# Kernel tuning notes

Hardware: AMD Instinct MI355X
Metric: run time of the kernel (lower is better)

## Reference

```python
import jax, jax.numpy as jnp
import numpy as np

B, N = 1, 768
C_S, C_Z, C_H, H, P_QK, P_V = 384, 128, 16, 12, 4, 8
INF = 100000.0
EPS = 1e-8


def _points(s, w, b, rot, trans, P):
    # PointProjection: linear -> [B,N,H,3,P] -> [B,N,H,P,3] local points,
    # then global = R @ p_local + t (rigid broadcast over heads/points).
    pl = (s @ w + b).reshape(s.shape[0], s.shape[1], H, 3, P)
    pl = jnp.moveaxis(pl, -2, -1)  # [B,N,H,P,3]
    return jnp.einsum('bnij,bnhpj->bnhpi', rot, pl) + trans[:, :, None, None, :]


def setup_inputs():
    key = jax.random.key(0)
    ks = jax.random.split(key, 14)

    def lin(k, fi, fo):
        k1, k2 = jax.random.split(k)
        w = jax.random.normal(k1, (fi, fo), jnp.float32) / np.float32(np.sqrt(fi))
        b = jax.random.normal(k2, (fo,), jnp.float32) * 0.01
        return w, b

    s = jax.random.normal(ks[0], (B, N, C_S), jnp.float32)
    z = jax.random.normal(ks[1], (B, N, N, C_Z), jnp.float32)
    rot = jnp.linalg.qr(jax.random.normal(ks[2], (B, N, 3, 3), jnp.float32))[0]
    trans = jax.random.normal(ks[3], (B, N, 3), jnp.float32)
    mask = jnp.ones((B, N), jnp.float32)

    w_q, b_q = lin(ks[4], C_S, H * C_H)
    w_k, b_k = lin(ks[5], C_S, H * C_H)
    w_v, b_v = lin(ks[6], C_S, H * C_H)
    w_qp, b_qp = lin(ks[7], C_S, H * 3 * P_QK)
    w_kp, b_kp = lin(ks[8], C_S, H * 3 * P_QK)
    w_vp, b_vp = lin(ks[9], C_S, H * 3 * P_V)
    w_b, b_b = lin(ks[10], C_Z, H)
    head_weights = jax.random.normal(ks[11], (H,), jnp.float32) * 0.1
    w_o, b_o = lin(ks[12], H * (C_Z + C_H + 4 * P_V), C_S)

    return dict(s=s, z=z, rot=rot, trans=trans, mask=mask,
                w_q=w_q, b_q=b_q, w_k=w_k, b_k=b_k, w_v=w_v, b_v=b_v,
                w_qp=w_qp, b_qp=b_qp, w_kp=w_kp, b_kp=b_kp, w_vp=w_vp, b_vp=b_vp,
                w_b=w_b, b_b=b_b, head_weights=head_weights, w_o=w_o, b_o=b_o)


def reference(s, z, rot, trans, mask,
              w_q, b_q, w_k, b_k, w_v, b_v,
              w_qp, b_qp, w_kp, b_kp, w_vp, b_vp,
              w_b, b_b, head_weights, w_o, b_o):
    # per-head point weights: sqrt(2 / (9 * P_QK)) * softplus(head_weights)
    pw = np.float32(np.sqrt(2.0 / (9.0 * P_QK))) * jnp.logaddexp(head_weights, 0.0)  # [H]

    q_pts = _points(s, w_qp, b_qp, rot, trans, P_QK)  # [B,N,H,P,3]
    k_pts = _points(s, w_kp, b_kp, rot, trans, P_QK)

    # sum_p ||q_p - k_p||^2 expanded: |q|^2 + |k|^2 - 2 q.k (summed over p,xyz)
    qk_pt = jnp.einsum('bqhpc,bkhpc->bqkh', q_pts, k_pts)
    q2 = jnp.sum(q_pts * q_pts, axis=(-2, -1))  # [B,N,H]
    k2 = jnp.sum(k_pts * k_pts, axis=(-2, -1))
    pt_att = -0.5 * pw * (q2[:, :, None, :] + k2[:, None, :, :] - 2.0 * qk_pt)  # [B,Nq,Nk,H]

    q = (s @ w_q + b_q).reshape(B, N, H, C_H) * np.float32(np.sqrt(1.0 / C_H))
    k = (s @ w_k + b_k).reshape(B, N, H, C_H)
    a = pt_att + jnp.einsum('bqhc,bkhc->bqkh', q, k)
    a = a + (z @ w_b + b_b)  # pair bias [B,Nq,Nk,H]

    sq_mask = mask[:, :, None] * mask[:, None, :]
    a = a + (INF * (sq_mask - 1.0))[..., None]
    a = jax.nn.softmax(a * np.float32(np.sqrt(1.0 / 3.0)), axis=-2)  # softmax over k

    v = (s @ w_v + b_v).reshape(B, N, H, C_H)
    o = jnp.einsum('bqkh,bkhc->bqhc', a, v).reshape(B, N, H * C_H)

    v_pts = _points(s, w_vp, b_vp, rot, trans, P_V)  # [B,N,H,P,3]
    o_pt = jnp.einsum('bqkh,bkhpc->bqhpc', a, v_pts).reshape(B, N, H * P_V, 3)
    # inverse rigid: R^T @ (p - t)
    o_pt = jnp.einsum('bnji,bnpj->bnpi', rot, o_pt - trans[:, :, None, :])  # [B,N,H*P_V,3]
    o_pt_norm = jnp.sqrt(jnp.sum(o_pt * o_pt, axis=-1) + EPS)  # [B,N,H*P_V]

    o_pair = jnp.einsum('bqkh,bqkc->bqhc', a, z).reshape(B, N, H * C_Z)

    cat = jnp.concatenate(
        [o, o_pt[..., 0], o_pt[..., 1], o_pt[..., 2], o_pt_norm, o_pair], axis=-1)
    return cat @ w_o + b_o  # [B,N,C_S]
```

## Files before the change

kernel.cpp:

```cpp
#include <hip/hip_runtime.h>
#include <math.h>

#define NN 768
#define KALL 1152
#define CATD 2112
#define INF_ 100000.0f
#define PACKN (385 * KALL)

__device__ __forceinline__ float4 ld4(const float* p) { return *(const float4*)p; }

__global__ __launch_bounds__(256) void pack_kernel(
    const float* wq, const float* bq, const float* wk, const float* bk,
    const float* wv, const float* bv, const float* wqp, const float* bqp,
    const float* wkp, const float* bkp, const float* wvp, const float* bvp,
    const float* wbm, float* Wall, float* ball, float* wtr) {
  int idx = blockIdx.x * 256 + threadIdx.x;
  if (idx >= PACKN + 1536) return;
  if (idx >= PACKN) {
    int u = idx - PACKN;
    int h = u >> 7, c = u & 127;
    wtr[u] = wbm[c * 12 + h];
    return;
  }
  int kk = idx / KALL, u = idx - kk * KALL;
  const float *w, *b; int col, dim; float sc = 1.f;
  if (u < 192)      { w = wq;  b = bq;  col = u;       dim = 192; sc = 0.25f; }
  else if (u < 384) { w = wk;  b = bk;  col = u - 192; dim = 192; }
  else if (u < 576) { w = wv;  b = bv;  col = u - 384; dim = 192; }
  else if (u < 720) { w = wqp; b = bqp; col = u - 576; dim = 144; }
  else if (u < 864) { w = wkp; b = bkp; col = u - 720; dim = 144; }
  else              { w = wvp; b = bvp; col = u - 864; dim = 288; }
  if (kk < 384) Wall[kk * KALL + u] = sc * w[kk * dim + col];
  else          ball[u] = sc * b[col];
}

__global__ __launch_bounds__(256) void proj_kernel(const float* s, const float* Wall,
                                                   const float* ball, float* proj) {
  int q0 = blockIdx.x * 32, c0 = blockIdx.y * 64;
  int tid = threadIdx.x;
  int qa = q0 + (tid >> 4) * 2, qb = qa + 1;
  int c = c0 + (tid & 15) * 4;
  const float* sa = s + qa * 384;
  const float* sb = s + qb * 384;
  const float* wp = Wall + c;
  float4 acc0 = {0, 0, 0, 0}, acc1 = {0, 0, 0, 0};
#pragma unroll 4
  for (int k = 0; k < 384; k++) {
    float4 w4 = ld4(wp + k * KALL);
    float a0 = sa[k], a1 = sb[k];
    acc0.x += a0 * w4.x; acc0.y += a0 * w4.y; acc0.z += a0 * w4.z; acc0.w += a0 * w4.w;
    acc1.x += a1 * w4.x; acc1.y += a1 * w4.y; acc1.z += a1 * w4.z; acc1.w += a1 * w4.w;
  }
  float4 b4 = ld4(ball + c);
  acc0.x += b4.x; acc0.y += b4.y; acc0.z += b4.z; acc0.w += b4.w;
  acc1.x += b4.x; acc1.y += b4.y; acc1.z += b4.z; acc1.w += b4.w;
  *(float4*)(proj + (size_t)qa * KALL + c) = acc0;
  *(float4*)(proj + (size_t)qb * KALL + c) = acc1;
}

__global__ __launch_bounds__(256) void points_kernel(const float* proj, const float* rot,
                                                     const float* trans, float* qpts, float* kpts,
                                                     float* vpts, float* q2, float* k2) {
  int n = blockIdx.x, tid = threadIdx.x;
  __shared__ float sq[12], sk[12];
  if (tid < 12) { sq[tid] = 0.f; sk[tid] = 0.f; }
  __syncthreads();
  if (tid < 192) {
    const float* R = rot + n * 9;
    const float* T = trans + n * 3;
    const float* pr = proj + (size_t)n * KALL;
    int base, P; float* outp; int h; bool isq = false, isk = false;
    if (tid < 48)      { h = tid >> 2; int p = tid & 3; base = 576 + h * 12; P = 4;
                         outp = qpts + n * 144 + h * 12 + p * 3; base += p; isq = true; }
    else if (tid < 96) { int i = tid - 48; h = i >> 2; int p = i & 3; base = 720 + h * 12; P = 4;
                         outp = kpts + n * 144 + h * 12 + p * 3; base += p; isk = true; }
    else               { int i = tid - 96; h = i >> 3; int p = i & 7; base = 864 + h * 24; P = 8;
                         outp = vpts + n * 288 + h * 24 + p * 3; base += p; }
    float l0 = pr[base], l1 = pr[base + P], l2 = pr[base + 2 * P];
    float g0 = R[0] * l0 + R[1] * l1 + R[2] * l2 + T[0];
    float g1 = R[3] * l0 + R[4] * l1 + R[5] * l2 + T[1];
    float g2 = R[6] * l0 + R[7] * l1 + R[8] * l2 + T[2];
    outp[0] = g0; outp[1] = g1; outp[2] = g2;
    float ns = g0 * g0 + g1 * g1 + g2 * g2;
    if (isq) atomicAdd(&sq[h], ns);
    else if (isk) atomicAdd(&sk[h], ns);
  }
  __syncthreads();
  if (tid < 12) { q2[n * 12 + tid] = sq[tid]; k2[n * 12 + tid] = sk[tid]; }
}

__global__ __launch_bounds__(256) void bias_kernel(const float* __restrict__ z,
                                                   const float* __restrict__ wtr,
                                                   const float* __restrict__ bb,
                                                   float* __restrict__ abuf) {
  int q = blockIdx.x, k0 = blockIdx.y * 96;
  int tid = threadIdx.x;
  int lane = tid & 63;
  int wv = tid >> 6;
  int grp = lane >> 5;
  int cl = lane & 31;
  __shared__ float lsm[96 * 100];

  float4 w4[12];
#pragma unroll
  for (int h = 0; h < 12; h++) w4[h] = ld4(wtr + h * 128 + cl * 4);

  const float* zq = z + ((size_t)q * NN + k0) * 128;
  int rbase = wv * 24;
  int quad = cl >> 2, sub = cl & 3;
#pragma unroll 2
  for (int it = 0; it < 12; it++) {
    int rloc = rbase + it * 2 + grp;
    float4 z4 = ld4(zq + (size_t)rloc * 128 + cl * 4);
    float a[12];
#pragma unroll
    for (int h = 0; h < 12; h++)
      a[h] = z4.x * w4[h].x + z4.y * w4[h].y + z4.z * w4[h].z + z4.w * w4[h].w;
#pragma unroll
    for (int h = 0; h < 12; h++) {
      a[h] += __shfl_xor(a[h], 1, 64);
      a[h] += __shfl_xor(a[h], 2, 64);
    }
    bool s1 = (sub == 1), s2 = (sub == 2);
    float vx = s1 ? a[4] : (s2 ? a[8]  : a[0]);
    float vy = s1 ? a[5] : (s2 ? a[9]  : a[1]);
    float vz = s1 ? a[6] : (s2 ? a[10] : a[2]);
    float vw = s1 ? a[7] : (s2 ? a[11] : a[3]);
    if (sub < 3) {
      float* p = lsm + rloc * 100 + quad * 12 + sub * 4;
      *(float4*)p = make_float4(vx, vy, vz, vw);
    }
  }
  __syncthreads();
  for (int i = tid; i < 96 * 12; i += 256) {
    int h = i / 96, k = i - h * 96;
    const float* p = lsm + k * 100 + h;
    float ssum = bb[h];
#pragma unroll
    for (int g = 0; g < 8; g++) ssum += p[g * 12];
    abuf[((size_t)q * 12 + h) * NN + k0 + k] = ssum;
  }
}

__global__ __launch_bounds__(256) void softmax_kernel(const float* proj, const float* qpts,
                                                      const float* kpts, const float* q2,
                                                      const float* k2, const float* mask,
                                                      const float* hw, float* abuf) {
  int q0 = blockIdx.x * 8, h = blockIdx.y;
  int tid = threadIdx.x;
  __shared__ float qw[8][16], qp[8][12], q2s[8], mq[8], red[4][8], row[8], pws;
  if (tid < 128) qw[tid >> 4][tid & 15] = proj[(size_t)(q0 + (tid >> 4)) * KALL + h * 16 + (tid & 15)];
  else if (tid < 224) { int i = tid - 128; qp[i / 12][i % 12] = qpts[(q0 + i / 12) * 144 + h * 12 + i % 12]; }
  else if (tid < 232) q2s[tid - 224] = q2[(q0 + tid - 224) * 12 + h];
  else if (tid < 240) mq[tid - 232] = mask[q0 + tid - 232];
  else if (tid == 240) {
    float x = hw[h];
    pws = 0.23570226039551584f * (fmaxf(x, 0.f) + log1pf(__expf(-fabsf(x))));
  }
  __syncthreads();

  float L[3][8];
#pragma unroll
  for (int i = 0; i < 3; i++) {
    int kk = i * 256 + tid;
    float kw[16], kp[12];
    const float* kwp = proj + (size_t)kk * KALL + 192 + h * 16;
    *(float4*)(kw) = ld4(kwp); *(float4*)(kw + 4) = ld4(kwp + 4);
    *(float4*)(kw + 8) = ld4(kwp + 8); *(float4*)(kw + 12) = ld4(kwp + 12);
    const float* kpp = kpts + (size_t)kk * 144 + h * 12;
    *(float4*)(kp) = ld4(kpp); *(float4*)(kp + 4) = ld4(kpp + 4); *(float4*)(kp + 8) = ld4(kpp + 8);
    float k2v = k2[kk * 12 + h];
    float mk = mask[kk];
#pragma unroll
    for (int q = 0; q < 8; q++) {
      float4 qa = *(const float4*)&qw[q][0];
      float4 qb = *(const float4*)&qw[q][4];
      float4 qc = *(const float4*)&qw[q][8];
      float4 qd = *(const float4*)&qw[q][12];
      float4 pa = *(const float4*)&qp[q][0];
      float4 pb = *(const float4*)&qp[q][4];
      float4 pc = *(const float4*)&qp[q][8];
      float d = qa.x * kw[0] + qa.y * kw[1] + qa.z * kw[2] + qa.w * kw[3]
              + qb.x * kw[4] + qb.y * kw[5] + qb.z * kw[6] + qb.w * kw[7]
              + qc.x * kw[8] + qc.y * kw[9] + qc.z * kw[10] + qc.w * kw[11]
              + qd.x * kw[12] + qd.y * kw[13] + qd.z * kw[14] + qd.w * kw[15];
      float dp = pa.x * kp[0] + pa.y * kp[1] + pa.z * kp[2] + pa.w * kp[3]
               + pb.x * kp[4] + pb.y * kp[5] + pb.z * kp[6] + pb.w * kp[7]
               + pc.x * kp[8] + pc.y * kp[9] + pc.z * kp[10] + pc.w * kp[11];
      float bias = abuf[((size_t)(q0 + q) * 12 + h) * NN + kk];
      float val = bias + d - 0.5f * pws * (q2s[q] + k2v - 2.f * dp) + INF_ * (mq[q] * mk - 1.f);
      L[i][q] = val * 0.5773502691896258f;
    }
  }
  float m[8];
#pragma unroll
  for (int q = 0; q < 8; q++) m[q] = fmaxf(fmaxf(L[0][q], L[1][q]), L[2][q]);
#pragma unroll
  for (int d = 1; d < 64; d <<= 1)
#pragma unroll
    for (int q = 0; q < 8; q++) m[q] = fmaxf(m[q], __shfl_xor(m[q], d, 64));
  int wv = tid >> 6;
  if ((tid & 63) == 0)
    for (int q = 0; q < 8; q++) red[wv][q] = m[q];
  __syncthreads();
  if (tid < 8) row[tid] = fmaxf(fmaxf(red[0][tid], red[1][tid]), fmaxf(red[2][tid], red[3][tid]));
  __syncthreads();
  float sm[8];
#pragma unroll
  for (int q = 0; q < 8; q++) {
    float mm = row[q];
    L[0][q] = __expf(L[0][q] - mm);
    L[1][q] = __expf(L[1][q] - mm);
    L[2][q] = __expf(L[2][q] - mm);
    sm[q] = L[0][q] + L[1][q] + L[2][q];
  }
#pragma unroll
  for (int d = 1; d < 64; d <<= 1)
#pragma unroll
    for (int q = 0; q < 8; q++) sm[q] += __shfl_xor(sm[q], d, 64);
  if ((tid & 63) == 0)
    for (int q = 0; q < 8; q++) red[wv][q] = sm[q];
  __syncthreads();
  if (tid < 8) row[tid] = 1.f / (red[0][tid] + red[1][tid] + red[2][tid] + red[3][tid]);
  __syncthreads();
#pragma unroll
  for (int q = 0; q < 8; q++) {
    float r = row[q];
    float* ap = abuf + ((size_t)(q0 + q) * 12 + h) * NN + tid;
    ap[0] = L[0][q] * r; ap[256] = L[1][q] * r; ap[512] = L[2][q] * r;
  }
}

__global__ __launch_bounds__(256) void opair_kernel(const float* z, const float* abuf, float* cat) {
  int q = blockIdx.x, tid = threadIdx.x;
  int c = tid & 127, h0 = tid >> 7;
  const float* zp = z + (size_t)q * NN * 128 + c;
  const float* ap = abuf + (size_t)q * 12 * NN;
  float acc[6] = {0, 0, 0, 0, 0, 0};
  for (int k4 = 0; k4 < NN; k4 += 4) {
    float4 av[6];
#pragma unroll
    for (int j = 0; j < 6; j++) av[j] = ld4(ap + (h0 + 2 * j) * NN + k4);
#pragma unroll
    for (int kk = 0; kk < 4; kk++) {
      float zv = zp[(size_t)(k4 + kk) * 128];
      const float* avf;
#pragma unroll
      for (int j = 0; j < 6; j++) {
        avf = (const float*)&av[j];
        acc[j] += zv * avf[kk];
      }
    }
  }
#pragma unroll
  for (int j = 0; j < 6; j++)
    cat[(size_t)q * CATD + 576 + (h0 + 2 * j) * 128 + c] = acc[j];
}

__global__ __launch_bounds__(256) void ovpart_kernel(const float* proj, const float* vpts,
                                                     const float* abuf, float* pov) {
  int h = blockIdx.x, q0 = blockIdx.y * 32, kz = blockIdx.z;
  int tid = threadIdx.x;
  int qg = tid >> 3, jb = tid & 7;
  int q = q0 + qg;
  const float* ap = abuf + ((size_t)q * 12 + h) * NN + kz * 192;
  const float* vp = proj + (size_t)(kz * 192) * KALL + 384 + h * 16;
  const float* vpp = vpts + (size_t)(kz * 192) * 288 + h * 24;
  float acc[5] = {0, 0, 0, 0, 0};
  for (int k = 0; k < 192; k += 4) {
    float4 a4 = ld4(ap + k);
    const float af[4] = {a4.x, a4.y, a4.z, a4.w};
#pragma unroll
    for (int kk = 0; kk < 4; kk++) {
      float av = af[kk];
      size_t kr = k + kk;
      acc[0] += av * vp[kr * KALL + jb];
      acc[1] += av * vp[kr * KALL + jb + 8];
      acc[2] += av * vpp[kr * 288 + jb];
      acc[3] += av * vpp[kr * 288 + jb + 8];
      acc[4] += av * vpp[kr * 288 + jb + 16];
    }
  }
  float* o = pov + (((size_t)kz * 768 + q) * 12 + h) * 40;
  o[jb] = acc[0]; o[jb + 8] = acc[1];
  o[16 + jb] = acc[2]; o[16 + jb + 8] = acc[3]; o[16 + jb + 16] = acc[4];
}

__global__ __launch_bounds__(256) void ovred_kernel(const float* pov, const float* rot,
                                                    const float* trans, float* cat) {
  int q = blockIdx.x, tid = threadIdx.x;
  const float* pq = pov + (size_t)q * 480;
  if (tid < 96) {
    int h = tid >> 3, p = tid & 7;
    float x = 0.f, y = 0.f, zz = 0.f;
#pragma unroll
    for (int j = 0; j < 4; j++) {
      const float* b = pq + (size_t)j * 768 * 480 + h * 40 + 16 + p * 3;
      x += b[0]; y += b[1]; zz += b[2];
    }
    const float* R = rot + q * 9;
    const float* T = trans + q * 3;
    float dx = x - T[0], dy = y - T[1], dz = zz - T[2];
    float lx = R[0] * dx + R[3] * dy + R[6] * dz;
    float ly = R[1] * dx + R[4] * dy + R[7] * dz;
    float lz = R[2] * dx + R[5] * dy + R[8] * dz;
    float nrm = sqrtf(lx * lx + ly * ly + lz * lz + 1e-8f);
    int hp = h * 8 + p;
    float* co = cat + (size_t)q * CATD;
    co[192 + hp] = lx; co[288 + hp] = ly; co[384 + hp] = lz; co[480 + hp] = nrm;
  } else {
    int i = tid - 96;
    int h = i >> 4, c = i & 15;
    float s = 0.f;
#pragma unroll
    for (int j = 0; j < 4; j++) s += pq[(size_t)j * 768 * 480 + h * 40 + c];
    cat[(size_t)q * CATD + h * 16 + c] = s;
    if (i < 32) {
      int i2 = i + 160;
      int h2 = i2 >> 4, c2 = i2 & 15;
      float s2 = 0.f;
#pragma unroll
      for (int j = 0; j < 4; j++) s2 += pq[(size_t)j * 768 * 480 + h2 * 40 + c2];
      cat[(size_t)q * CATD + h2 * 16 + c2] = s2;
    }
  }
}

__global__ __launch_bounds__(256) void out_part_kernel(const float* cat, const float* wo,
                                                       float* part) {
  int q0 = blockIdx.x * 16, c0 = blockIdx.y * 64, k0 = blockIdx.z * 264;
  int tid = threadIdx.x;
  int q = q0 + (tid >> 4);
  int c = c0 + (tid & 15) * 4;
  const float* cp = cat + (size_t)q * CATD + k0;
  const float* wp = wo + (size_t)k0 * 384 + c;
  float4 acc = {0, 0, 0, 0};
#pragma unroll 8
  for (int k = 0; k < 264; k++) {
    float a = cp[k];
    float4 w4 = ld4(wp + (size_t)k * 384);
    acc.x += a * w4.x; acc.y += a * w4.y; acc.z += a * w4.z; acc.w += a * w4.w;
  }
  *(float4*)(part + ((size_t)blockIdx.z * 768 + q) * 384 + c) = acc;
}

__global__ __launch_bounds__(256) void out_reduce_kernel(const float* part, const float* bo,
                                                         float* out) {
  int idx = blockIdx.x * 256 + threadIdx.x;
  int q = idx / 96, cg = idx - q * 96;
  int c = cg * 4;
  float4 acc = ld4(bo + c);
#pragma unroll
  for (int j = 0; j < 8; j++) {
    float4 p = ld4(part + ((size_t)j * 768 + q) * 384 + c);
    acc.x += p.x; acc.y += p.y; acc.z += p.z; acc.w += p.w;
  }
  *(float4*)(out + (size_t)q * 384 + c) = acc;
}

extern "C" void kernel_launch(void* const* d_in, const int* in_sizes, int n_in,
                              void* d_out, int out_size, void* d_ws, size_t ws_size,
                              hipStream_t stream) {
  const float* s     = (const float*)d_in[0];
  const float* z     = (const float*)d_in[1];
  const float* rot   = (const float*)d_in[2];
  const float* trans = (const float*)d_in[3];
  const float* mask  = (const float*)d_in[4];
  const float* wq    = (const float*)d_in[5];
  const float* bq    = (const float*)d_in[6];
  const float* wk    = (const float*)d_in[7];
  const float* bk    = (const float*)d_in[8];
  const float* wv    = (const float*)d_in[9];
  const float* bv    = (const float*)d_in[10];
  const float* wqp   = (const float*)d_in[11];
  const float* bqp   = (const float*)d_in[12];
  const float* wkp   = (const float*)d_in[13];
  const float* bkp   = (const float*)d_in[14];
  const float* wvp   = (const float*)d_in[15];
  const float* bvp   = (const float*)d_in[16];
  const float* wb    = (const float*)d_in[17];
  const float* bb    = (const float*)d_in[18];
  const float* hw    = (const float*)d_in[19];
  const float* wo    = (const float*)d_in[20];
  const float* bo    = (const float*)d_in[21];
  float* out = (float*)d_out;

  float* ws = (float*)d_ws;
  float* proj  = ws;
  float* Wall  = proj + 884736;
  float* ball  = Wall + 442368;
  float* qpts  = ball + 1152;
  float* kpts  = qpts + 110592;
  float* vpts  = kpts + 110592;
  float* q2    = vpts + 221184;
  float* k2    = q2 + 9216;
  float* abuf  = k2 + 9216;
  float* cat   = abuf + 7077888;
  float* part  = cat + 1622016;
  float* wtr   = part + 2359296;
  float* pov   = wtr + 2048;

  pack_kernel<<<dim3((PACKN + 1536 + 255) / 256), 256, 0, stream>>>(
      wq, bq, wk, bk, wv, bv, wqp, bqp, wkp, bkp, wvp, bvp, wb, Wall, ball, wtr);
  proj_kernel<<<dim3(24, 18), 256, 0, stream>>>(s, Wall, ball, proj);
  points_kernel<<<dim3(768), 256, 0, stream>>>(proj, rot, trans, qpts, kpts, vpts, q2, k2);
  bias_kernel<<<dim3(768, 8), 256, 0, stream>>>(z, wtr, bb, abuf);
  softmax_kernel<<<dim3(96, 12), 256, 0, stream>>>(proj, qpts, kpts, q2, k2, mask, hw, abuf);
  opair_kernel<<<dim3(768), 256, 0, stream>>>(z, abuf, cat);
  ovpart_kernel<<<dim3(12, 24, 4), 256, 0, stream>>>(proj, vpts, abuf, pov);
  ovred_kernel<<<dim3(768), 256, 0, stream>>>(pov, rot, trans, cat);
  out_part_kernel<<<dim3(48, 6, 8), 256, 0, stream>>>(cat, wo, part);
  out_reduce_kernel<<<dim3(288), 256, 0, stream>>>(part, bo, out);
}
```

Measured before the change: 873.3 us.

## Restructure opair kernel with float4 z loads, split-K over warps, and DPP reductions

The opair kernel previously had each thread read scalar z values and accumulate 6 heads for one channel. It now has each of 8 warps cover a 96-row slice of k, load z as float4 across 4 channels, and accumulate all 12 heads. Partial sums are combined through about 49 KB of shared memory. The bias kernel swaps its shuffle-xor quad reductions for DPP moves and adds a minimum-occupancy launch bound. The new layout cuts redundant z loads and improves load width, at the cost of higher register pressure (48 accumulators) and large shared-memory use that may limit occupancy.

```diff
diff --git a/kernel.cpp b/kernel.cpp
--- a/kernel.cpp
+++ b/kernel.cpp
@@ -8,6 +8,12 @@
 #define PACKN (385 * KALL)
 
 __device__ __forceinline__ float4 ld4(const float* p) { return *(const float4*)p; }
+
+__device__ __forceinline__ float qsum_dpp(float v) {
+  v += __int_as_float(__builtin_amdgcn_mov_dpp(__float_as_int(v), 0xB1, 0xF, 0xF, true));
+  v += __int_as_float(__builtin_amdgcn_mov_dpp(__float_as_int(v), 0x4E, 0xF, 0xF, true));
+  return v;
+}
 
 __global__ __launch_bounds__(256) void pack_kernel(
     const float* wq, const float* bq, const float* wk, const float* bk,
@@ -89,10 +95,10 @@
   if (tid < 12) { q2[n * 12 + tid] = sq[tid]; k2[n * 12 + tid] = sk[tid]; }
 }
 
-__global__ __launch_bounds__(256) void bias_kernel(const float* __restrict__ z,
-                                                   const float* __restrict__ wtr,
-                                                   const float* __restrict__ bb,
-                                                   float* __restrict__ abuf) {
+__global__ __launch_bounds__(256, 4) void bias_kernel(const float* __restrict__ z,
+                                                      const float* __restrict__ wtr,
+                                                      const float* __restrict__ bb,
+                                                      float* __restrict__ abuf) {
   int q = blockIdx.x, k0 = blockIdx.y * 96;
   int tid = threadIdx.x;
   int lane = tid & 63;
@@ -117,10 +123,7 @@
     for (int h = 0; h < 12; h++)
       a[h] = z4.x * w4[h].x + z4.y * w4[h].y + z4.z * w4[h].z + z4.w * w4[h].w;
 #pragma unroll
-    for (int h = 0; h < 12; h++) {
-      a[h] += __shfl_xor(a[h], 1, 64);
-      a[h] += __shfl_xor(a[h], 2, 64);
-    }
+    for (int h = 0; h < 12; h++) a[h] = qsum_dpp(a[h]);
     bool s1 = (sub == 1), s2 = (sub == 2);
     float vx = s1 ? a[4] : (s2 ? a[8]  : a[0]);
     float vy = s1 ? a[5] : (s2 ? a[9]  : a[1]);
@@ -231,30 +234,44 @@
   }
 }
 
-__global__ __launch_bounds__(256) void opair_kernel(const float* z, const float* abuf, float* cat) {
+__global__ __launch_bounds__(256) void opair_kernel(const float* __restrict__ z,
+                                                    const float* __restrict__ abuf,
+                                                    float* __restrict__ cat) {
   int q = blockIdx.x, tid = threadIdx.x;
-  int c = tid & 127, h0 = tid >> 7;
-  const float* zp = z + (size_t)q * NN * 128 + c;
-  const float* ap = abuf + (size_t)q * 12 * NN;
-  float acc[6] = {0, 0, 0, 0, 0, 0};
-  for (int k4 = 0; k4 < NN; k4 += 4) {
-    float4 av[6];
-#pragma unroll
-    for (int j = 0; j < 6; j++) av[j] = ld4(ap + (h0 + 2 * j) * NN + k4);
-#pragma unroll
-    for (int kk = 0; kk < 4; kk++) {
-      float zv = zp[(size_t)(k4 + kk) * 128];
-      const float* avf;
-#pragma unroll
-      for (int j = 0; j < 6; j++) {
-        avf = (const float*)&av[j];
-        acc[j] += zv * avf[kk];
-      }
-    }
-  }
-#pragma unroll
-  for (int j = 0; j < 6; j++)
-    cat[(size_t)q * CATD + 576 + (h0 + 2 * j) * 128 + c] = acc[j];
+  int cq = tid & 31;
+  int g  = tid >> 5;
+  __shared__ float red[8 * 1540];
+  const float* zp = z + ((size_t)q * NN + g * 96) * 128 + cq * 4;
+  const float* ap = abuf + (size_t)q * 12 * NN + g * 96;
+  float acc[12][4];
+#pragma unroll
+  for (int h = 0; h < 12; h++) { acc[h][0] = 0.f; acc[h][1] = 0.f; acc[h][2] = 0.f; acc[h][3] = 0.f; }
+  for (int r = 0; r < 96; r += 4) {
+    float4 z0 = ld4(zp + (size_t)(r + 0) * 128);
+    float4 z1 = ld4(zp + (size_t)(r + 1) * 128);
+    float4 z2 = ld4(zp + (size_t)(r + 2) * 128);
+    float4 z3 = ld4(zp + (size_t)(r + 3) * 128);
+#pragma unroll
+    for (int h = 0; h < 12; h++) {
+      float4 a4 = ld4(ap + h * NN + r);
+      acc[h][0] += a4.x * z0.x + a4.y * z1.x + a4.z * z2.x + a4.w * z3.x;
+      acc[h][1] += a4.x * z0.y + a4.y * z1.y + a4.z * z2.y + a4.w * z3.y;
+      acc[h][2] += a4.x * z0.z + a4.y * z1.z + a4.z * z2.z + a4.w * z3.z;
+      acc[h][3] += a4.x * z0.w + a4.y * z1.w + a4.z * z2.w + a4.w * z3.w;
+    }
+  }
+#pragma unroll
+  for (int h = 0; h < 12; h++)
+    *(float4*)(red + g * 1540 + h * 128 + cq * 4) = *(float4*)acc[h];
+  __syncthreads();
+#pragma unroll
+  for (int i = 0; i < 6; i++) {
+    int idx = i * 256 + tid;
+    float ssum = 0.f;
+#pragma unroll
+    for (int gg = 0; gg < 8; gg++) ssum += red[gg * 1540 + idx];
+    cat[(size_t)q * CATD + 576 + idx] = ssum;
+  }
 }
 
 __global__ __launch_bounds__(256) void ovpart_kernel(const float* proj, const float* vpts,
```

Result: faster. 766.0 us (-12.3%).
